# Kernel optimization log

Measured on AMD Instinct MI355X. Metric: run time of the kernel, lower is better.

Reference implementation:

```python
import jax, jax.numpy as jnp
import numpy as np

EPS = 1e-7
B, C, IMG = 1024, 3, 32
NCLASS = 10
N_IN, L_IN, L_OUT = 64, 16, 16   # primary caps: 64 capsules of length 16; digit caps length 16
R_ITER = 3


def squash(c, axis):
    dot = jnp.sum(c * c, axis=axis, keepdims=True)
    return dot / (1.0 + dot) / jnp.sqrt(dot + EPS) * c


def conv2d(x, w, b, stride):
    y = jax.lax.conv_general_dilated(x, w, (stride, stride), 'VALID',
                                     dimension_numbers=('NCHW', 'OIHW', 'NCHW'))
    return y + b[None, :, None, None]


def setup_inputs() -> dict:
    key = jax.random.key(0)
    ks = jax.random.split(key, 16)
    inp = {
        'x': jax.random.uniform(ks[0], (B, C, IMG, IMG), dtype=jnp.float32),
        'y': jax.random.randint(ks[1], (B,), 0, NCLASS, dtype=jnp.int64),
        'conv1_w': 0.05 * jax.random.normal(ks[2], (128, C, 3, 3), jnp.float32),
        'conv1_b': jnp.zeros((128,), jnp.float32),
        'conv2_w': 0.05 * jax.random.normal(ks[3], (256, 128, 5, 5), jnp.float32),
        'conv2_b': jnp.zeros((256,), jnp.float32),
        'conv3_w': 0.05 * jax.random.normal(ks[4], (256, 256, 5, 5), jnp.float32),
        'conv3_b': jnp.zeros((256,), jnp.float32),
        'caps_w': 0.05 * jax.random.normal(ks[5], (N_IN, NCLASS, L_IN, L_OUT), jnp.float32),
        'caps_b': 0.05 * jax.random.normal(ks[6], (NCLASS, L_OUT), jnp.float32),
        'fc1_w': 0.05 * jax.random.normal(ks[7], (512, NCLASS * L_OUT), jnp.float32),
        'fc1_b': jnp.zeros((512,), jnp.float32),
        'fc2_w': 0.05 * jax.random.normal(ks[8], (1024, 512), jnp.float32),
        'fc2_b': jnp.zeros((1024,), jnp.float32),
        'fc3_w': 0.05 * jax.random.normal(ks[9], (IMG * IMG * C, 1024), jnp.float32),
        'fc3_b': jnp.zeros((IMG * IMG * C,), jnp.float32),
    }
    return inp


def reference(x, y, conv1_w, conv1_b, conv2_w, conv2_b, conv3_w, conv3_b,
              caps_w, caps_b, fc1_w, fc1_b, fc2_w, fc2_b, fc3_w, fc3_b):
    # CNN blocks
    h = jax.nn.relu(conv2d(x, conv1_w, conv1_b, 2))   # [B,128,15,15]
    h = jax.nn.relu(conv2d(h, conv2_w, conv2_b, 2))   # [B,256,6,6]
    h = jax.nn.relu(conv2d(h, conv3_w, conv3_b, 1))   # [B,256,2,2]

    # Primary capsules: [B,64,16], squashed along capsule-length axis
    prim = squash(h.reshape(h.shape[0], N_IN, L_IN), axis=-1)

    # u_hat[b,i,o,j] = sum_k W[i,o,k,j] * prim[b,i,k]  -> [B,64,10,16]
    u_hat = jnp.einsum('bik,iokj->bioj', prim, caps_w)
    u_hat_det = jax.lax.stop_gradient(u_hat)

    b_ij = jnp.zeros((h.shape[0], N_IN, NCLASS), dtype=u_hat.dtype)
    v = None
    for r in range(R_ITER):
        c_ij = jax.nn.softmax(b_ij, axis=2)           # over output capsules
        uh = u_hat if r == R_ITER - 1 else u_hat_det
        s = jnp.einsum('bio,bioj->boj', c_ij, uh) + caps_b   # [B,10,16]
        v = squash(s, axis=-1)
        if r < R_ITER - 1:
            agree = jnp.einsum('bioj,boj->bio', u_hat_det, jax.lax.stop_gradient(v))
            b_ij = b_ij + agree

    # capsule lengths: [B,10,1,1]
    v_lengths = jnp.sqrt(jnp.sum(v * v, axis=-1, keepdims=True) + EPS)[..., None]

    # reconstruction (mask by true label one-hot)
    one_hot = jax.nn.one_hot(y, NCLASS, dtype=v.dtype)       # [B,10]
    masked = (v * one_hot[:, :, None]).reshape(v.shape[0], NCLASS * L_OUT)
    h1 = jax.nn.relu(masked @ fc1_w.T + fc1_b)
    h2 = jax.nn.relu(h1 @ fc2_w.T + fc2_b)
    decoded = jax.nn.sigmoid(h2 @ fc3_w.T + fc3_b)           # [B,3072]
    return (v_lengths, decoded)
```

## Files before the change

### kernel.cpp

```cpp
#include <hip/hip_runtime.h>
#include <hip/hip_bf16.h>
#include <math.h>

#define EPSF 1e-7f

typedef __attribute__((ext_vector_type(8))) short bhalf8;
typedef __attribute__((ext_vector_type(4))) float floatx4;

__global__ __launch_bounds__(256) void conv1_kernel(
    const float* __restrict__ x, const float* __restrict__ w,
    const float* __restrict__ bias, __hip_bfloat16* __restrict__ out)
{
  const int b = blockIdx.x;
  const int t = threadIdx.x;
  if (t >= 225) return;
  const int py = t / 15, px = t % 15;
  const float* xb = x + b * 3072;
  float win[27];
#pragma unroll
  for (int c = 0; c < 3; ++c)
#pragma unroll
    for (int ky = 0; ky < 3; ++ky)
#pragma unroll
      for (int kx = 0; kx < 3; ++kx)
        win[c*9 + ky*3 + kx] = xb[c*1024 + (py*2 + ky)*32 + (px*2 + kx)];
#pragma unroll 1
  for (int oc0 = 0; oc0 < 128; oc0 += 32) {
    __hip_bfloat16 hv[32];
#pragma unroll
    for (int oc = 0; oc < 32; ++oc) {
      const float* wp = &w[(oc0 + oc)*27];
      float acc = bias[oc0 + oc];
#pragma unroll
      for (int q = 0; q < 27; ++q) acc = fmaf(win[q], wp[q], acc);
      hv[oc] = __float2bfloat16(fmaxf(acc, 0.f));
    }
    uint4* dst = (uint4*)&out[((size_t)b*225 + t)*128 + oc0];
    const uint4* src = (const uint4*)hv;
#pragma unroll
    for (int q = 0; q < 4; ++q) dst[q] = src[q];
  }
}

__global__ __launch_bounds__(256) void prep_kernel(
    const float* __restrict__ conv2w, const float* __restrict__ conv3w,
    const float* __restrict__ capsw,  const float* __restrict__ fc1w,
    const float* __restrict__ fc2w,   const float* __restrict__ fc3w,
    __hip_bfloat16* __restrict__ wt2, __hip_bfloat16* __restrict__ wt3,
    __hip_bfloat16* __restrict__ cwt, float* __restrict__ fc1wt,
    __hip_bfloat16* __restrict__ wf2, __hip_bfloat16* __restrict__ wf3)
{
  const int t = threadIdx.x;
  int b = blockIdx.x;
  if (b < 12288) {
    int i = b*256 + t;
    wf3[i] = __float2bfloat16(fc3w[i]);
    return;
  }
  b -= 12288;
  if (b < 6400) {
    int i = b*256 + t;
    int s = i >> 14, r = i & 16383;
    int oc = r >> 6, kq = r & 63;
    int k = s*64 + kq;
    int tap = k >> 8, ic = k & 255;
    wt3[i] = __float2bfloat16(conv3w[(oc*256 + ic)*25 + tap]);
    return;
  }
  b -= 6400;
  if (b < 3200) {
    int i = b*256 + t;
    int s = i >> 13, r = i & 8191;
    int oc = r >> 5, kq = r & 31;
    int h = (s >= 50) ? 1 : 0;
    int r2 = s - h*50;
    int tap = r2 >> 1, q = r2 & 1;
    int ic = h*64 + q*32 + kq;
    wt2[i] = __float2bfloat16(conv2w[(oc*128 + ic)*25 + tap]);
    return;
  }
  b -= 3200;
  if (b < 2048) {
    int i = b*256 + t;
    wf2[i] = __float2bfloat16(fc2w[i]);
    return;
  }
  b -= 2048;
  if (b < 640) {
    int i2 = b*256 + t;
    int k = i2 & 15, j = (i2 >> 4) & 15, io = i2 >> 8;
    cwt[i2] = __float2bfloat16(capsw[(io*16 + k)*16 + j]);
    return;
  }
  b -= 640;
  {
    int i = b*256 + t;
    int j = i >> 9, n = i & 511;
    fc1wt[i] = fc1w[n*160 + j];
  }
}

__global__ __launch_bounds__(512) void conv2_mfma_kernel(
    const __hip_bfloat16* __restrict__ a,
    const __hip_bfloat16* __restrict__ wt,
    const float* __restrict__ bias,
    __hip_bfloat16* __restrict__ out)
{
  __shared__ __align__(16) unsigned short Il[4*225*64];
  const int b0   = blockIdx.x * 4;
  const int t    = threadIdx.x;
  const int lane = t & 63;
  const int w    = t >> 6;
  const int wm   = w >> 2;
  const int wn   = w & 3;
  const int n    = lane & 15;
  const int g    = lane >> 4;

  const char* gB = (const char*)wt + (wn*64 + n)*64 + g*16;
  bhalf8 bs0[4], bs1[4];
#pragma unroll
  for (int nt = 0; nt < 4; ++nt) {
    bs0[nt] = *(const bhalf8*)(gB + nt*1024);
    bs1[nt] = *(const bhalf8*)(gB + 16384 + nt*1024);
  }

  int Abase[5], em[5];
#pragma unroll
  for (int mt = 0; mt < 5; ++mt) {
    int tile = wm*5 + mt;
    int m = tile*16 + n;
    if (m >= 144) m = 0;
    int img = m / 36, pos = m - img*36;
    int py = pos / 6, px = pos - py*6;
    int pixb = 30*py + 2*px;
    Abase[mt] = (img*225 + pixb) * 128;
    em[mt] = g + m;
  }

  floatx4 acc[5][4];
#pragma unroll
  for (int mt = 0; mt < 5; ++mt)
#pragma unroll
    for (int nt = 0; nt < 4; ++nt)
      acc[mt][nt] = (floatx4){0.f, 0.f, 0.f, 0.f};

  int s = 0;
#pragma unroll 1
  for (int h = 0; h < 2; ++h) {
    if (h) __syncthreads();
    for (int i = t; i < 7200; i += 512) {
      int img = i / 1800;
      int r = i - img*1800;
      int p = r >> 3, c = r & 7;
      uint4 v = *(const uint4*)((const char*)a +
                ((size_t)(b0+img)*225 + p)*256 + h*128 + c*16);
      int px15 = p % 15, py15 = p / 15;
      int csw = (c + (px15 >> 1) + 6*(py15 >> 1) + ((img & 1) << 2)) & 7;
      *(uint4*)((char*)Il + (img*225 + p)*128 + csw*16) = v;
    }
    __syncthreads();

    int dpix = 0, kx = 0, ky = 0;
#pragma unroll 1
    for (int tap = 0; tap < 25; ++tap) {
      const int doff = dpix << 7;
      const int dsw  = (kx >> 1) + 6*(ky >> 1);
      int a0[5];
#pragma unroll
      for (int mt = 0; mt < 5; ++mt)
        a0[mt] = Abase[mt] + doff + (((em[mt] + dsw) & 7) << 4);

#pragma unroll
      for (int mt = 0; mt < 4; ++mt) {
        bhalf8 av = *(const bhalf8*)((const char*)Il + a0[mt]);
#pragma unroll
        for (int nt = 0; nt < 4; ++nt)
          acc[mt][nt] = __builtin_amdgcn_mfma_f32_16x16x32_bf16(av, bs0[nt], acc[mt][nt], 0, 0, 0);
      }
      if (wm == 0) {
        bhalf8 av = *(const bhalf8*)((const char*)Il + a0[4]);
#pragma unroll
        for (int nt = 0; nt < 4; ++nt)
          acc[4][nt] = __builtin_amdgcn_mfma_f32_16x16x32_bf16(av, bs0[nt], acc[4][nt], 0, 0, 0);
      }
      {
        const int spre = (s + 2 < 100) ? (s + 2) : 99;
#pragma unroll
        for (int nt = 0; nt < 4; ++nt)
          bs0[nt] = *(const bhalf8*)(gB + (size_t)spre*16384 + nt*1024);
      }
#pragma unroll
      for (int mt = 0; mt < 4; ++mt) {
        bhalf8 av = *(const bhalf8*)((const char*)Il + (a0[mt] ^ 64));
#pragma unroll
        for (int nt = 0; nt < 4; ++nt)
          acc[mt][nt] = __builtin_amdgcn_mfma_f32_16x16x32_bf16(av, bs1[nt], acc[mt][nt], 0, 0, 0);
      }
      if (wm == 0) {
        bhalf8 av = *(const bhalf8*)((const char*)Il + (a0[4] ^ 64));
#pragma unroll
        for (int nt = 0; nt < 4; ++nt)
          acc[4][nt] = __builtin_amdgcn_mfma_f32_16x16x32_bf16(av, bs1[nt], acc[4][nt], 0, 0, 0);
      }
      {
        const int spre = (s + 3 < 100) ? (s + 3) : 99;
#pragma unroll
        for (int nt = 0; nt < 4; ++nt)
          bs1[nt] = *(const bhalf8*)(gB + (size_t)spre*16384 + nt*1024);
      }
      s += 2;
      if (kx == 4) { kx = 0; ++ky; dpix += 11; } else { ++kx; ++dpix; }
    }
  }

  float bv[4];
#pragma unroll
  for (int nt = 0; nt < 4; ++nt) bv[nt] = bias[wn*64 + nt*16 + n];
#pragma unroll
  for (int mt = 0; mt < 5; ++mt) {
    if (mt < 4 || wm == 0) {
      int tile = wm*5 + mt;
#pragma unroll
      for (int r = 0; r < 4; ++r) {
        int m = tile*16 + g*4 + r;
        int img = m / 36, pos = m - img*36;
        size_t o = (((size_t)(b0+img)*36 + pos) << 8) + wn*64 + n;
#pragma unroll
        for (int nt = 0; nt < 4; ++nt)
          out[o + nt*16] = __float2bfloat16(fmaxf(acc[mt][nt][r] + bv[nt], 0.f));
      }
    }
  }
}

__global__ __launch_bounds__(512) void conv3_mfma_kernel(
    const __hip_bfloat16* __restrict__ a,
    const __hip_bfloat16* __restrict__ wt,
    float* __restrict__ pout)
{
  __shared__ __align__(16) unsigned short Il[16*1448];
  const int b0   = blockIdx.x * 16;
  const int kq   = blockIdx.y;
  const int t    = threadIdx.x;
  const int lane = t & 63;
  const int w    = t >> 6;
  const int n    = lane & 15;
  const int g    = lane >> 4;

  for (int i = t; i < 2304; i += 512) {
    int img = i / 144, r = i - img*144;
    int p = r >> 2, c = r & 3;
    uint4 v = *(const uint4*)((const char*)a +
              ((((size_t)(b0+img)*36 + p) << 9) + kq*64 + c*16));
    *(uint4*)((char*)Il + (img*1448 + p*40 + c*8)*2) = v;
  }

  const char* gB = (const char*)wt + (size_t)(w*32 + n)*128 +
                   (kq & 1)*64 + g*16;
  const int kqs = kq >> 1;
  bhalf8 b00, b01, b10, b11;
  b00 = *(const bhalf8*)(gB + (size_t)(0*4 + kqs)*32768);
  b01 = *(const bhalf8*)(gB + (size_t)(0*4 + kqs)*32768 + 2048);
  b10 = *(const bhalf8*)(gB + (size_t)(1*4 + kqs)*32768);
  b11 = *(const bhalf8*)(gB + (size_t)(1*4 + kqs)*32768 + 2048);

  const int d = n >> 2, pos = n & 3;
  const int pb = (pos >> 1)*6 + (pos & 1);
  int ab[4];
#pragma unroll
  for (int mt = 0; mt < 4; ++mt)
    ab[mt] = ((mt*4 + d)*1448 + pb*40 + g*8) * 2;

  floatx4 acc[4][2];
#pragma unroll
  for (int mt = 0; mt < 4; ++mt)
#pragma unroll
    for (int nt = 0; nt < 2; ++nt)
      acc[mt][nt] = (floatx4){0.f, 0.f, 0.f, 0.f};

  __syncthreads();

  int toff = 0, kx = 0;
#pragma unroll 1
  for (int tap = 0; tap < 24; tap += 2) {
#pragma unroll
    for (int mt = 0; mt < 4; ++mt) {
      bhalf8 av = *(const bhalf8*)((const char*)Il + ab[mt] + toff*80);
      acc[mt][0] = __builtin_amdgcn_mfma_f32_16x16x32_bf16(av, b00, acc[mt][0], 0, 0, 0);
      acc[mt][1] = __builtin_amdgcn_mfma_f32_16x16x32_bf16(av, b01, acc[mt][1], 0, 0, 0);
    }
    b00 = *(const bhalf8*)(gB + (size_t)((tap+2)*4 + kqs)*32768);
    b01 = *(const bhalf8*)(gB + (size_t)((tap+2)*4 + kqs)*32768 + 2048);
    if (++kx == 5) { kx = 0; toff += 2; } else ++toff;
#pragma unroll
    for (int mt = 0; mt < 4; ++mt) {
      bhalf8 av = *(const bhalf8*)((const char*)Il + ab[mt] + toff*80);
      acc[mt][0] = __builtin_amdgcn_mfma_f32_16x16x32_bf16(av, b10, acc[mt][0], 0, 0, 0);
      acc[mt][1] = __builtin_amdgcn_mfma_f32_16x16x32_bf16(av, b11, acc[mt][1], 0, 0, 0);
    }
    {
      const int tpre = (tap + 3 <= 24) ? (tap + 3) : 24;
      b10 = *(const bhalf8*)(gB + (size_t)(tpre*4 + kqs)*32768);
      b11 = *(const bhalf8*)(gB + (size_t)(tpre*4 + kqs)*32768 + 2048);
    }
    if (++kx == 5) { kx = 0; toff += 2; } else ++toff;
  }
#pragma unroll
  for (int mt = 0; mt < 4; ++mt) {
    bhalf8 av = *(const bhalf8*)((const char*)Il + ab[mt] + toff*80);
    acc[mt][0] = __builtin_amdgcn_mfma_f32_16x16x32_bf16(av, b00, acc[mt][0], 0, 0, 0);
    acc[mt][1] = __builtin_amdgcn_mfma_f32_16x16x32_bf16(av, b01, acc[mt][1], 0, 0, 0);
  }

  float* po = pout + (size_t)kq*1048576;
#pragma unroll
  for (int mt = 0; mt < 4; ++mt) {
#pragma unroll
    for (int r = 0; r < 4; ++r) {
      int m = mt*16 + g*4 + r;
      int img = m >> 2, p2 = m & 3;
#pragma unroll
      for (int nt = 0; nt < 2; ++nt)
        po[((size_t)(b0+img)*256 + w*32 + nt*16 + n)*4 + p2] = acc[mt][nt][r];
    }
  }
}

__global__ __launch_bounds__(256) void caps_kernel(
    const float* __restrict__ pout, const __hip_bfloat16* __restrict__ cwt,
    const float* __restrict__ cb, const float* __restrict__ c3b,
    const int* __restrict__ y,
    const float* __restrict__ fc1wt, const float* __restrict__ fc1b,
    float* __restrict__ vlen, __hip_bfloat16* __restrict__ h1f)
{
  __shared__ float prim[1024];
  __shared__ float uh[10240];
  __shared__ float bij[640];
  __shared__ float cij[640];
  __shared__ float vv[160];
  const int b = blockIdx.x, t = threadIdx.x;
  {
    const float* pp = pout + (size_t)b*1024 + t*4;
    float4 s4 = *(const float4*)pp;
#pragma unroll
    for (int q = 1; q < 8; ++q) {
      float4 v = *(const float4*)(pp + (size_t)q*1048576);
      s4.x += v.x; s4.y += v.y; s4.z += v.z; s4.w += v.w;
    }
    const float bv = c3b[t];
    float4 h = make_float4(fmaxf(s4.x + bv, 0.f), fmaxf(s4.y + bv, 0.f),
                           fmaxf(s4.z + bv, 0.f), fmaxf(s4.w + bv, 0.f));
    float dd = h.x*h.x + h.y*h.y + h.z*h.z + h.w*h.w;
    dd += __shfl_xor(dd, 1);
    dd += __shfl_xor(dd, 2);
    float sc = dd / (1.f + dd) / sqrtf(dd + EPSF);
    float4 o4 = make_float4(h.x*sc, h.y*sc, h.z*sc, h.w*sc);
    *(float4*)&prim[t*4] = o4;
  }
  for (int f = t; f < 640; f += 256) bij[f] = 0.f;
  __syncthreads();
  for (int f = t; f < 10240; f += 256) {
    const int i = f / 160;
    const uint4* wv = (const uint4*)(cwt + (size_t)f*16);
    uint4 wa = wv[0], wb = wv[1];
    unsigned uw[8] = {wa.x, wa.y, wa.z, wa.w, wb.x, wb.y, wb.z, wb.w};
    const float* pp = prim + i*16;
    float s = 0.f;
#pragma unroll
    for (int q = 0; q < 8; ++q) {
      float lo = __uint_as_float(uw[q] << 16);
      float hi = __uint_as_float(uw[q] & 0xffff0000u);
      s = fmaf(pp[2*q],   lo, s);
      s = fmaf(pp[2*q+1], hi, s);
    }
    uh[f] = s;
  }
  __syncthreads();
  for (int r = 0; r < 3; ++r) {
    if (t < 64) {
      float e[10];
      float mx = -1e30f;
#pragma unroll
      for (int o = 0; o < 10; ++o) { e[o] = bij[t*10 + o]; mx = fmaxf(mx, e[o]); }
      float sum = 0.f;
#pragma unroll
      for (int o = 0; o < 10; ++o) { e[o] = expf(e[o] - mx); sum += e[o]; }
      float inv = 1.f / sum;
#pragma unroll
      for (int o = 0; o < 10; ++o) cij[t*10 + o] = e[o] * inv;
    }
    __syncthreads();
    if (t < 160) {
      const int o = t >> 4;
      float s0 = cb[t], s1 = 0.f, s2 = 0.f, s3 = 0.f;
      for (int i = 0; i < 64; i += 4) {
        s0 = fmaf(cij[(i+0)*10 + o], uh[(i+0)*160 + t], s0);
        s1 = fmaf(cij[(i+1)*10 + o], uh[(i+1)*160 + t], s1);
        s2 = fmaf(cij[(i+2)*10 + o], uh[(i+2)*160 + t], s2);
        s3 = fmaf(cij[(i+3)*10 + o], uh[(i+3)*160 + t], s3);
      }
      float s = (s0 + s1) + (s2 + s3);
      float dd = s*s;
      dd += __shfl_xor(dd, 1); dd += __shfl_xor(dd, 2);
      dd += __shfl_xor(dd, 4); dd += __shfl_xor(dd, 8);
      float sc = dd / (1.f + dd) / sqrtf(dd + EPSF);
      vv[t] = s * sc;
      if (r == 2 && (t & 15) == 0)
        vlen[b*10 + o] = sqrtf(sc*sc*dd + EPSF);
    }
    __syncthreads();
    if (r < 2) {
      for (int f = t; f < 640; f += 256) {
        int i = f / 10, o = f % 10;
        const float* up = &uh[i*160 + o*16];
        const float* vp = &vv[o*16];
        float a = 0.f;
#pragma unroll
        for (int j = 0; j < 16; ++j) a = fmaf(up[j], vp[j], a);
        bij[f] += a;
      }
      __syncthreads();
    }
  }
  const int yb = y[b];
  const float* vy = &vv[yb*16];
  for (int nn = t; nn < 512; nn += 256) {
    float s = fc1b[nn];
#pragma unroll
    for (int k = 0; k < 16; ++k)
      s = fmaf(vy[k], fc1wt[(yb*16 + k)*512 + nn], s);
    h1f[b*512 + nn] = __float2bfloat16(fmaxf(s, 0.f));
  }
}

template<int ACT, int MT, int NT>
__global__ __launch_bounds__(256) void fc_mfma_kernel(
    const __hip_bfloat16* __restrict__ A,
    const __hip_bfloat16* __restrict__ W,
    const float* __restrict__ bias,
    void* __restrict__ outv, int M, int N, int K)
{
  const int t    = threadIdx.x;
  const int lane = t & 63;
  const int w    = t >> 6;
  const int wr   = w >> 1, wc = w & 1;
  const int n    = lane & 15, g = lane >> 4;
  const int m0   = blockIdx.x * (2*MT*16) + wr*(MT*16);
  const int n0   = blockIdx.y * (2*NT*16) + wc*(NT*16);
  const __hip_bfloat16* Ap = A + (size_t)(m0 + n)*K + g*8;
  const __hip_bfloat16* Wp = W + (size_t)(n0 + n)*K + g*8;
  const int steps = K >> 5;

  bhalf8 aa0[MT], aa1[MT], bb0[NT], bb1[NT];
#pragma unroll
  for (int mt = 0; mt < MT; ++mt) {
    aa0[mt] = *(const bhalf8*)(Ap + (size_t)mt*16*K);
    aa1[mt] = *(const bhalf8*)(Ap + (size_t)mt*16*K + 32);
  }
#pragma unroll
  for (int nt = 0; nt < NT; ++nt) {
    bb0[nt] = *(const bhalf8*)(Wp + (size_t)nt*16*K);
    bb1[nt] = *(const bhalf8*)(Wp + (size_t)nt*16*K + 32);
  }

  floatx4 acc[MT][NT];
#pragma unroll
  for (int mt = 0; mt < MT; ++mt)
#pragma unroll
    for (int nt = 0; nt < NT; ++nt)
      acc[mt][nt] = (floatx4){0.f, 0.f, 0.f, 0.f};

#pragma unroll 1
  for (int s = 0; s < steps; s += 2) {
#pragma unroll
    for (int mt = 0; mt < MT; ++mt)
#pragma unroll
      for (int nt = 0; nt < NT; ++nt)
        acc[mt][nt] = __builtin_amdgcn_mfma_f32_16x16x32_bf16(
            aa0[mt], bb0[nt], acc[mt][nt], 0, 0, 0);
    {
      const int spre = (s + 2 < steps) ? (s + 2) : s;
#pragma unroll
      for (int mt = 0; mt < MT; ++mt)
        aa0[mt] = *(const bhalf8*)(Ap + (size_t)mt*16*K + spre*32);
#pragma unroll
      for (int nt = 0; nt < NT; ++nt)
        bb0[nt] = *(const bhalf8*)(Wp + (size_t)nt*16*K + spre*32);
    }
#pragma unroll
    for (int mt = 0; mt < MT; ++mt)
#pragma unroll
      for (int nt = 0; nt < NT; ++nt)
        acc[mt][nt] = __builtin_amdgcn_mfma_f32_16x16x32_bf16(
            aa1[mt], bb1[nt], acc[mt][nt], 0, 0, 0);
    {
      const int spre = (s + 3 < steps) ? (s + 3) : (s + 1);
#pragma unroll
      for (int mt = 0; mt < MT; ++mt)
        aa1[mt] = *(const bhalf8*)(Ap + (size_t)mt*16*K + spre*32);
#pragma unroll
      for (int nt = 0; nt < NT; ++nt)
        bb1[nt] = *(const bhalf8*)(Wp + (size_t)nt*16*K + spre*32);
    }
  }

#pragma unroll
  for (int mt = 0; mt < MT; ++mt) {
#pragma unroll
    for (int r = 0; r < 4; ++r) {
      const int m = m0 + mt*16 + g*4 + r;
#pragma unroll
      for (int nt = 0; nt < NT; ++nt) {
        const int col = n0 + nt*16 + n;
        float v = acc[mt][nt][r] + bias[col];
        if (ACT == 0) {
          ((__hip_bfloat16*)outv)[(size_t)m*N + col] =
              __float2bfloat16(fmaxf(v, 0.f));
        } else {
          ((float*)outv)[(size_t)m*N + col] = 1.f / (1.f + expf(-v));
        }
      }
    }
  }
}

extern "C" void kernel_launch(void* const* d_in, const int* in_sizes, int n_in,
                              void* d_out, int out_size, void* d_ws, size_t ws_size,
                              hipStream_t stream) {
  const float* x       = (const float*)d_in[0];
  const int*   y       = (const int*)  d_in[1];
  const float* conv1_w = (const float*)d_in[2];
  const float* conv1_b = (const float*)d_in[3];
  const float* conv2_w = (const float*)d_in[4];
  const float* conv2_b = (const float*)d_in[5];
  const float* conv3_w = (const float*)d_in[6];
  const float* conv3_b = (const float*)d_in[7];
  const float* caps_w  = (const float*)d_in[8];
  const float* caps_b  = (const float*)d_in[9];
  const float* fc1_w   = (const float*)d_in[10];
  const float* fc1_b   = (const float*)d_in[11];
  const float* fc2_w   = (const float*)d_in[12];
  const float* fc2_b   = (const float*)d_in[13];
  const float* fc3_w   = (const float*)d_in[14];
  const float* fc3_b   = (const float*)d_in[15];
  float* out = (float*)d_out;
  float* ws  = (float*)d_ws;

  __hip_bfloat16* h1t   = (__hip_bfloat16*)ws;
  __hip_bfloat16* wt2   = (__hip_bfloat16*)(ws + 14745600);
  __hip_bfloat16* wt3   = (__hip_bfloat16*)(ws + 15155200);
  __hip_bfloat16* h2t   = (__hip_bfloat16*)(ws + 15974400);
  float*          pout  = ws + 20692992;
  __hip_bfloat16* h1f   = (__hip_bfloat16*)(ws + 29081600);
  __hip_bfloat16* h2f   = (__hip_bfloat16*)(ws + 29343744);
  __hip_bfloat16* wf2   = (__hip_bfloat16*)(ws + 29868032);
  __hip_bfloat16* wf3   = (__hip_bfloat16*)(ws + 30130176);
  __hip_bfloat16* cwt   = (__hip_bfloat16*)(ws + 31703040);
  float*          fc1wt = ws + 31784960;

  prep_kernel<<<dim3(24896), 256, 0, stream>>>(
      conv2_w, conv3_w, caps_w, fc1_w, fc2_w, fc3_w,
      wt2, wt3, cwt, fc1wt, wf2, wf3);
  conv1_kernel<<<dim3(1024),       256, 0, stream>>>(x, conv1_w, conv1_b, h1t);
  conv2_mfma_kernel<<<dim3(256),   512, 0, stream>>>(h1t, wt2, conv2_b, h2t);
  conv3_mfma_kernel<<<dim3(64, 8), 512, 0, stream>>>(h2t, wt3, pout);
  caps_kernel<<<dim3(1024),        256, 0, stream>>>(pout, cwt, caps_b, conv3_b,
                                                     y, fc1wt, fc1_b, out, h1f);
  fc_mfma_kernel<0,2,2><<<dim3(16, 16), 256, 0, stream>>>(
      h1f, wf2, fc2_b, h2f, 1024, 1024, 512);
  fc_mfma_kernel<1,2,2><<<dim3(16, 48), 256, 0, stream>>>(
      h2f, wf3, fc3_b, out + 10240, 1024, 3072, 1024);
}
```

Baseline: 352.8 us.

## Stage conv1 weights and output in LDS; double conv2 waves per block

conv1 now loads its weights and bias into shared memory, padded to 28 per channel so they can be read as float4. Its bf16 output is staged in a swizzled LDS buffer and written out with fully coalesced 16-byte stores, replacing the strided per-thread global stores. conv2 is launched with 1024 threads (16 waves) instead of 512. The 9 M-tiles are split so the first row of waves takes 3 tiles and the others take 2, which shortens each wave's MFMA chain and improves latency hiding. The trade-offs are higher register pressure under launch_bounds(1024), and every wave still reloads the B fragments from global memory.

```diff
diff --git a/kernel.cpp b/kernel.cpp
--- a/kernel.cpp
+++ b/kernel.cpp
@@ -11,34 +11,65 @@
     const float* __restrict__ x, const float* __restrict__ w,
     const float* __restrict__ bias, __hip_bfloat16* __restrict__ out)
 {
+  __shared__ float wl[3584];
+  __shared__ float bl[128];
+  __shared__ __align__(16) unsigned short ob[225*128];
   const int b = blockIdx.x;
   const int t = threadIdx.x;
-  if (t >= 225) return;
-  const int py = t / 15, px = t % 15;
-  const float* xb = x + b * 3072;
-  float win[27];
-#pragma unroll
-  for (int c = 0; c < 3; ++c)
-#pragma unroll
-    for (int ky = 0; ky < 3; ++ky)
-#pragma unroll
-      for (int kx = 0; kx < 3; ++kx)
-        win[c*9 + ky*3 + kx] = xb[c*1024 + (py*2 + ky)*32 + (px*2 + kx)];
+  for (int i = t; i < 3584; i += 256) {
+    int oc = i / 28, q = i - oc*28;
+    wl[i] = (q < 27) ? w[oc*27 + q] : 0.f;
+  }
+  if (t < 128) bl[t] = bias[t];
+
+  float win[28];
+  win[27] = 0.f;
+  if (t < 225) {
+    const int py = t / 15, px = t % 15;
+    const float* xb = x + b * 3072;
+#pragma unroll
+    for (int c = 0; c < 3; ++c)
+#pragma unroll
+      for (int ky = 0; ky < 3; ++ky)
+#pragma unroll
+        for (int kx = 0; kx < 3; ++kx)
+          win[c*9 + ky*3 + kx] = xb[c*1024 + (py*2 + ky)*32 + (px*2 + kx)];
+  }
+  __syncthreads();
+
+  if (t < 225) {
 #pragma unroll 1
-  for (int oc0 = 0; oc0 < 128; oc0 += 32) {
-    __hip_bfloat16 hv[32];
-#pragma unroll
-    for (int oc = 0; oc < 32; ++oc) {
-      const float* wp = &w[(oc0 + oc)*27];
-      float acc = bias[oc0 + oc];
-#pragma unroll
-      for (int q = 0; q < 27; ++q) acc = fmaf(win[q], wp[q], acc);
-      hv[oc] = __float2bfloat16(fmaxf(acc, 0.f));
-    }
-    uint4* dst = (uint4*)&out[((size_t)b*225 + t)*128 + oc0];
-    const uint4* src = (const uint4*)hv;
-#pragma unroll
-    for (int q = 0; q < 4; ++q) dst[q] = src[q];
+    for (int oc0 = 0; oc0 < 128; oc0 += 32) {
+      __hip_bfloat16 hv[32];
+#pragma unroll
+      for (int oc = 0; oc < 32; ++oc) {
+        const float4* wp = (const float4*)&wl[(oc0 + oc)*28];
+        float acc = bl[oc0 + oc];
+#pragma unroll
+        for (int qq = 0; qq < 7; ++qq) {
+          float4 wv = wp[qq];
+          acc = fmaf(win[qq*4 + 0], wv.x, acc);
+          acc = fmaf(win[qq*4 + 1], wv.y, acc);
+          acc = fmaf(win[qq*4 + 2], wv.z, acc);
+          acc = fmaf(win[qq*4 + 3], wv.w, acc);
+        }
+        hv[oc] = __float2bfloat16(fmaxf(acc, 0.f));
+      }
+      const uint4* src = (const uint4*)hv;
+#pragma unroll
+      for (int q = 0; q < 4; ++q) {
+        int c = (oc0 >> 3) + q;
+        int slot = (c + t) & 15;
+        *(uint4*)((char*)ob + t*256 + slot*16) = src[q];
+      }
+    }
+  }
+  __syncthreads();
+
+  for (int idx = t; idx < 3600; idx += 256) {
+    int p = idx >> 4, c = idx & 15;
+    uint4 v = *(const uint4*)((const char*)ob + p*256 + (((c + p) & 15) << 4));
+    *(uint4*)((char*)out + (size_t)b*57600 + idx*16) = v;
   }
 }
 
@@ -100,7 +131,7 @@
   }
 }
 
-__global__ __launch_bounds__(512) void conv2_mfma_kernel(
+__global__ __launch_bounds__(1024) void conv2_mfma_kernel(
     const __hip_bfloat16* __restrict__ a,
     const __hip_bfloat16* __restrict__ wt,
     const float* __restrict__ bias,
@@ -124,12 +155,14 @@
     bs1[nt] = *(const bhalf8*)(gB + 16384 + nt*1024);
   }
 
-  int Abase[5], em[5];
-#pragma unroll
-  for (int mt = 0; mt < 5; ++mt) {
-    int tile = wm*5 + mt;
+  const int tbase = (wm == 0) ? 0 : (wm*2 + 1);
+  const int MTW   = (wm == 0) ? 3 : 2;
+  int Abase[3], em[3];
+#pragma unroll
+  for (int mt = 0; mt < 3; ++mt) {
+    int tile = tbase + mt;
     int m = tile*16 + n;
-    if (m >= 144) m = 0;
+    if (mt >= MTW) m = 0;
     int img = m / 36, pos = m - img*36;
     int py = pos / 6, px = pos - py*6;
     int pixb = 30*py + 2*px;
@@ -137,9 +170,9 @@
     em[mt] = g + m;
   }
 
-  floatx4 acc[5][4];
-#pragma unroll
-  for (int mt = 0; mt < 5; ++mt)
+  floatx4 acc[3][4];
+#pragma unroll
+  for (int mt = 0; mt < 3; ++mt)
 #pragma unroll
     for (int nt = 0; nt < 4; ++nt)
       acc[mt][nt] = (floatx4){0.f, 0.f, 0.f, 0.f};
@@ -148,7 +181,7 @@
 #pragma unroll 1
   for (int h = 0; h < 2; ++h) {
     if (h) __syncthreads();
-    for (int i = t; i < 7200; i += 512) {
+    for (int i = t; i < 7200; i += 1024) {
       int img = i / 1800;
       int r = i - img*1800;
       int p = r >> 3, c = r & 7;
@@ -165,23 +198,23 @@
     for (int tap = 0; tap < 25; ++tap) {
       const int doff = dpix << 7;
       const int dsw  = (kx >> 1) + 6*(ky >> 1);
-      int a0[5];
-#pragma unroll
-      for (int mt = 0; mt < 5; ++mt)
+      int a0[3];
+#pragma unroll
+      for (int mt = 0; mt < 3; ++mt)
         a0[mt] = Abase[mt] + doff + (((em[mt] + dsw) & 7) << 4);
 
 #pragma unroll
-      for (int mt = 0; mt < 4; ++mt) {
+      for (int mt = 0; mt < 2; ++mt) {
         bhalf8 av = *(const bhalf8*)((const char*)Il + a0[mt]);
 #pragma unroll
         for (int nt = 0; nt < 4; ++nt)
           acc[mt][nt] = __builtin_amdgcn_mfma_f32_16x16x32_bf16(av, bs0[nt], acc[mt][nt], 0, 0, 0);
       }
       if (wm == 0) {
-        bhalf8 av = *(const bhalf8*)((const char*)Il + a0[4]);
+        bhalf8 av = *(const bhalf8*)((const char*)Il + a0[2]);
 #pragma unroll
         for (int nt = 0; nt < 4; ++nt)
-          acc[4][nt] = __builtin_amdgcn_mfma_f32_16x16x32_bf16(av, bs0[nt], acc[4][nt], 0, 0, 0);
+          acc[2][nt] = __builtin_amdgcn_mfma_f32_16x16x32_bf16(av, bs0[nt], acc[2][nt], 0, 0, 0);
       }
       {
         const int spre = (s + 2 < 100) ? (s + 2) : 99;
@@ -190,17 +223,17 @@
           bs0[nt] = *(const bhalf8*)(gB + (size_t)spre*16384 + nt*1024);
       }
 #pragma unroll
-      for (int mt = 0; mt < 4; ++mt) {
+      for (int mt = 0; mt < 2; ++mt) {
         bhalf8 av = *(const bhalf8*)((const char*)Il + (a0[mt] ^ 64));
 #pragma unroll
         for (int nt = 0; nt < 4; ++nt)
           acc[mt][nt] = __builtin_amdgcn_mfma_f32_16x16x32_bf16(av, bs1[nt], acc[mt][nt], 0, 0, 0);
       }
       if (wm == 0) {
-        bhalf8 av = *(const bhalf8*)((const char*)Il + (a0[4] ^ 64));
+        bhalf8 av = *(const bhalf8*)((const char*)Il + (a0[2] ^ 64));
 #pragma unroll
         for (int nt = 0; nt < 4; ++nt)
-          acc[4][nt] = __builtin_amdgcn_mfma_f32_16x16x32_bf16(av, bs1[nt], acc[4][nt], 0, 0, 0);
+          acc[2][nt] = __builtin_amdgcn_mfma_f32_16x16x32_bf16(av, bs1[nt], acc[2][nt], 0, 0, 0);
       }
       {
         const int spre = (s + 3 < 100) ? (s + 3) : 99;
@@ -217,9 +250,9 @@
 #pragma unroll
   for (int nt = 0; nt < 4; ++nt) bv[nt] = bias[wn*64 + nt*16 + n];
 #pragma unroll
-  for (int mt = 0; mt < 5; ++mt) {
-    if (mt < 4 || wm == 0) {
-      int tile = wm*5 + mt;
+  for (int mt = 0; mt < 3; ++mt) {
+    if (mt < 2 || wm == 0) {
+      int tile = tbase + mt;
 #pragma unroll
       for (int r = 0; r < 4; ++r) {
         int m = tile*16 + g*4 + r;
@@ -562,7 +595,7 @@
       conv2_w, conv3_w, caps_w, fc1_w, fc2_w, fc3_w,
       wt2, wt3, cwt, fc1wt, wf2, wf3);
   conv1_kernel<<<dim3(1024),       256, 0, stream>>>(x, conv1_w, conv1_b, h1t);
-  conv2_mfma_kernel<<<dim3(256),   512, 0, stream>>>(h1t, wt2, conv2_b, h2t);
+  conv2_mfma_kernel<<<dim3(256),  1024, 0, stream>>>(h1t, wt2, conv2_b, h2t);
   conv3_mfma_kernel<<<dim3(64, 8), 512, 0, stream>>>(h2t, wt3, pout);
   caps_kernel<<<dim3(1024),        256, 0, stream>>>(pout, cwt, caps_b, conv3_b,
                                                      y, fc1wt, fc1_b, out, h1f);
```

Result: slower. 413.4 us (+17.2%).
